# Performance work log

Hardware: AMD Instinct MI355X
Metric: run time of the kernel (lower is better)

Reference implementation:

```python
import jax, jax.numpy as jnp
import numpy as np


def setup_inputs() -> dict:
    key = jax.random.key(0)
    k1, k2 = jax.random.split(key)
    x = jax.random.normal(k1, (32, 128, 56, 56), dtype=jnp.float32)
    weight = jax.random.normal(k2, (256, 128, 3, 3), dtype=jnp.float32) * 0.01
    bias = jnp.zeros((256,), dtype=jnp.float32)
    return {"x": x, "weight": weight, "bias": bias}


def reference(x, weight, bias):
    # Faithful to Conv2dGEMM: im2col + GEMM is mathematically a standard
    # cross-correlation conv with the given stride/padding. We express it as
    # the efficient fused form (implicit GEMM) which computes identical math.
    stride, padding = 1, 1
    out = jax.lax.conv_general_dilated(
        x, weight,
        window_strides=(stride, stride),
        padding=[(padding, padding), (padding, padding)],
        dimension_numbers=("NCHW", "OIHW", "NCHW"),
    )  # [B, out_ch, H_out, W_out]
    return out + bias[None, :, None, None]
```

## Files before the change

kernel.cpp:

```cpp
#include <hip/hip_runtime.h>
#include <stdint.h>

typedef __bf16 bf16x8 __attribute__((ext_vector_type(8)));
typedef float  f32x4  __attribute__((ext_vector_type(4)));

#define NB   32
#define CI   128
#define HH   56
#define WW   56
#define CO   256
#define HP   58
#define HW   (HH*WW)
#define MTOT (NB*HW)
#define KTOT 1152

#define XT_ELEMS ((size_t)NB*HP*HP*CI)
#define XT_BYTES (XT_ELEMS*2)
#define WT_BYTES ((size_t)CO*KTOT*2)
#define CTR_OFF  (XT_BYTES + WT_BYTES)

#define XPOSE_BLOCKS (NB*HH)
#define WX_BLOCKS    ((CO*KTOT)/256)
#define HALO_BLOCKS  ((NB*228*16)/256)

__global__ void prep_kernel(const float* __restrict__ x, const float* __restrict__ wg,
                            __bf16* __restrict__ xt, __bf16* __restrict__ wt,
                            unsigned* __restrict__ ctr) {
  __shared__ float tile[CI][57];
  int bx = blockIdx.x, t = threadIdx.x;
  if (bx == 0 && t == 0) *ctr = 0u;
  if (bx < XPOSE_BLOCKS) {
    int n = bx / HH, h = bx % HH;
    const float* src = x + (size_t)n * CI * HW + (size_t)h * WW;
    for (int idx = t; idx < CI * 14; idx += 256) {
      int c = idx / 14, w4 = idx - c * 14;
      float4 v = *(const float4*)(src + (size_t)c * HW + w4 * 4);
      tile[c][w4 * 4 + 0] = v.x;
      tile[c][w4 * 4 + 1] = v.y;
      tile[c][w4 * 4 + 2] = v.z;
      tile[c][w4 * 4 + 3] = v.w;
    }
    __syncthreads();
    __bf16* dst = xt + ((size_t)(n * HP + h + 1) * HP + 1) * CI;
    for (int idx = t; idx < WW * 16; idx += 256) {
      int w = idx >> 4, c8 = (idx & 15) * 8;
      bf16x8 v;
      for (int k = 0; k < 8; ++k) v[k] = (__bf16)tile[c8 + k][w];
      *(bf16x8*)(dst + (size_t)w * CI + c8) = v;
    }
  } else if (bx < XPOSE_BLOCKS + WX_BLOCKS) {
    int id = (bx - XPOSE_BLOCKS) * 256 + t;
    int o = id / KTOT;
    int k = id - o * KTOT;
    int rs = k >> 7, c = k & 127;
    wt[id] = (__bf16)wg[(size_t)o * KTOT + c * 9 + rs];
  } else {
    int id = (bx - XPOSE_BLOCKS - WX_BLOCKS) * 256 + t;
    int chunk = id & 15;
    int p = (id >> 4) % 228;
    int n = id / (228 * 16);
    int h, w;
    if (p < 58)       { h = 0;           w = p; }
    else if (p < 116) { h = 57;          w = p - 58; }
    else if (p < 172) { h = p - 116 + 1; w = 0; }
    else              { h = p - 172 + 1; w = 57; }
    int4* dst = (int4*)(xt + ((size_t)(n * HP + h) * HP + w) * CI) + chunk;
    *dst = make_int4(0, 0, 0, 0);
  }
}

#define BM 128
#define BN 256
#define NKT 18
#define NTILES (MTOT/BM)

#define STAGE_A2(BS, OFF) \
  { _Pragma("unroll") for (int i_ = 0; i_ < 2; ++i_) \
      __builtin_amdgcn_global_load_lds( \
        (const __attribute__((address_space(1))) void*)(xtc + baseA[i_] + (OFF)), \
        (__attribute__((address_space(3))) void*)(lds + (BS)*16384 + i_*8192 + ldst), 16, 0, 0); }

#define STAGE_B01(BS, OFF) \
  { _Pragma("unroll") for (int i_ = 0; i_ < 2; ++i_) \
      __builtin_amdgcn_global_load_lds( \
        (const __attribute__((address_space(1))) void*)(wtc + baseB[i_] + (OFF)), \
        (__attribute__((address_space(3))) void*)(lds + 49152 + (BS)*32768 + i_*8192 + ldst), 16, 0, 0); }

#define STAGE_B23(BS, OFF) \
  { _Pragma("unroll") for (int i_ = 2; i_ < 4; ++i_) \
      __builtin_amdgcn_global_load_lds( \
        (const __attribute__((address_space(1))) void*)(wtc + baseB[i_] + (OFF)), \
        (__attribute__((address_space(3))) void*)(lds + 49152 + (BS)*32768 + i_*8192 + ldst), 16, 0, 0); }

#define KBODY(KT, BC, BS, DOSTAGE, DOBAR, VMCLIT) do { \
  int kt2_ = (KT) + 2; \
  int rs2_ = kt2_ >> 1; int r2_ = (rs2_*11) >> 5; int s2_ = rs2_ - 3*r2_; \
  uint32_t offA2_ = (uint32_t)((r2_*HP + s2_) * 256 + (kt2_ & 1) * 128); \
  uint32_t offB2_ = (uint32_t)(kt2_ * 128); \
  const char* Ab_ = lds + (BC)*16384; \
  const char* Bb_ = lds + 49152 + (BC)*32768; \
  bf16x8 av_[4][2], bva_[2][2], bvb_[2][2]; \
  _Pragma("unroll") for (int a_ = 0; a_ < 4; ++a_) { \
    av_[a_][0] = *(const bf16x8*)(Ab_ + rowA + a_*2048 + slot0); \
    av_[a_][1] = *(const bf16x8*)(Ab_ + rowA + a_*2048 + slot1); } \
  _Pragma("unroll") for (int b_ = 0; b_ < 2; ++b_) { \
    bva_[b_][0] = *(const bf16x8*)(Bb_ + rowB + b_*2048 + slot0); \
    bva_[b_][1] = *(const bf16x8*)(Bb_ + rowB + b_*2048 + slot1); } \
  if (DOSTAGE) { STAGE_A2(BS, offA2_); STAGE_B01(BS, offB2_); } \
  __builtin_amdgcn_s_setprio(1); \
  _Pragma("unroll") for (int a_ = 0; a_ < 4; ++a_) { \
    _Pragma("unroll") for (int b_ = 0; b_ < 2; ++b_) { \
      acc[a_][b_] = __builtin_amdgcn_mfma_f32_16x16x32_bf16(av_[a_][0], bva_[b_][0], acc[a_][b_], 0, 0, 0); \
      acc[a_][b_] = __builtin_amdgcn_mfma_f32_16x16x32_bf16(av_[a_][1], bva_[b_][1], acc[a_][b_], 0, 0, 0); } } \
  __builtin_amdgcn_s_setprio(0); \
  _Pragma("unroll") for (int b_ = 0; b_ < 2; ++b_) { \
    bvb_[b_][0] = *(const bf16x8*)(Bb_ + rowB + 4096 + b_*2048 + slot0); \
    bvb_[b_][1] = *(const bf16x8*)(Bb_ + rowB + 4096 + b_*2048 + slot1); } \
  if (DOSTAGE) { STAGE_B23(BS, offB2_); } \
  __builtin_amdgcn_s_setprio(1); \
  _Pragma("unroll") for (int a_ = 0; a_ < 4; ++a_) { \
    _Pragma("unroll") for (int b_ = 0; b_ < 2; ++b_) { \
      acc[a_][b_+2] = __builtin_amdgcn_mfma_f32_16x16x32_bf16(av_[a_][0], bvb_[b_][0], acc[a_][b_+2], 0, 0, 0); \
      acc[a_][b_+2] = __builtin_amdgcn_mfma_f32_16x16x32_bf16(av_[a_][1], bvb_[b_][1], acc[a_][b_+2], 0, 0, 0); } } \
  __builtin_amdgcn_s_setprio(0); \
  if (DOBAR) { \
    asm volatile("s_waitcnt vmcnt(" VMCLIT ")" ::: "memory"); \
    __builtin_amdgcn_sched_barrier(0); \
    __builtin_amdgcn_s_barrier(); \
    __builtin_amdgcn_sched_barrier(0); } \
} while (0)

__global__ __launch_bounds__(512, 2) void conv_gemm(
    const __bf16* __restrict__ xt, const __bf16* __restrict__ wt,
    const float* __restrict__ bias, float* __restrict__ out,
    unsigned* __restrict__ ctr) {
  __shared__ char lds[147456];
  __shared__ int sh_mb;
  int t = threadIdx.x;
  const char* xtc = (const char*)xt;
  const char* wtc = (const char*)wt;

  int arow = t >> 3;
  int kbsrc = ((t & 7) * 16) ^ ((arow & 7) << 4);
  int ldst = t * 16;
  uint32_t baseB[4];
#pragma unroll
  for (int i = 0; i < 4; ++i)
    baseB[i] = (i * 64 + arow) * (KTOT * 2) + kbsrc;

  int wid = t >> 6, lane = t & 63;
  int wm = (wid >> 2) * 64;
  int wn = (wid & 3) * 64;
  int lr = lane & 15, hi = lane >> 4;
  int swz = (lr & 7) << 4;
  int slot0 = (hi * 16) ^ swz;
  int slot1 = (64 + hi * 16) ^ swz;
  int rowA = (wm + lr) * 128;
  int rowB = (wn + lr) * 128;

  for (;;) {
    if (t == 0) sh_mb = (int)atomicAdd(ctr, 1u);
    __syncthreads();
    int mb = sh_mb;
    if (mb >= NTILES) break;

    uint32_t baseA[2];
#pragma unroll
    for (int i = 0; i < 2; ++i) {
      unsigned m = mb * BM + i * 64 + arow;
      unsigned nimg = m / HW;
      unsigned hw = m - nimg * HW;
      unsigned h = hw / WW;
      unsigned w = hw - h * WW;
      baseA[i] = ((nimg * HP + h) * HP + w) * (CI * 2) + kbsrc;
    }

    f32x4 acc[4][4];
#pragma unroll
    for (int i = 0; i < 4; ++i)
#pragma unroll
      for (int j = 0; j < 4; ++j) acc[i][j] = (f32x4){0.f, 0.f, 0.f, 0.f};

    STAGE_A2(0, 0u);   STAGE_B01(0, 0u);   STAGE_B23(0, 0u);
    STAGE_A2(1, 128u); STAGE_B01(1, 128u); STAGE_B23(1, 128u);
    asm volatile("s_waitcnt vmcnt(6)" ::: "memory");
    __builtin_amdgcn_sched_barrier(0);
    __builtin_amdgcn_s_barrier();
    __builtin_amdgcn_sched_barrier(0);

    for (int kt = 0; kt < 15; kt += 3) {
      KBODY(kt + 0, 0, 2, 1, 1, "6");
      KBODY(kt + 1, 1, 0, 1, 1, "6");
      KBODY(kt + 2, 2, 1, 1, 1, "6");
    }
    KBODY(15, 0, 2, 1, 1, "6");
    KBODY(16, 1, 0, 0, 1, "0");
    KBODY(17, 2, 1, 0, 0, "0");

#pragma unroll
    for (int j = 0; j < 4; ++j) {
      int o = wn + j * 16 + lr;
      float bv = bias[o];
#pragma unroll
      for (int i = 0; i < 4; ++i) {
        unsigned m0 = mb * BM + wm + i * 16 + hi * 4;
        unsigned nimg = m0 / HW;
        unsigned hw = m0 - nimg * HW;
        f32x4 v = acc[i][j];
        v[0] += bv; v[1] += bv; v[2] += bv; v[3] += bv;
        *(f32x4*)(out + ((size_t)nimg * CO + o) * HW + hw) = v;
      }
    }
  }
}

extern "C" void kernel_launch(void* const* d_in, const int* in_sizes, int n_in,
                              void* d_out, int out_size, void* d_ws, size_t ws_size,
                              hipStream_t stream) {
  const float* x    = (const float*)d_in[0];
  const float* wg   = (const float*)d_in[1];
  const float* bias = (const float*)d_in[2];
  float* out = (float*)d_out;

  __bf16* xt = (__bf16*)d_ws;
  __bf16* wt = (__bf16*)((char*)d_ws + XT_BYTES);
  unsigned* ctr = (unsigned*)((char*)d_ws + CTR_OFF);

  prep_kernel<<<XPOSE_BLOCKS + WX_BLOCKS + HALO_BLOCKS, 256, 0, stream>>>(x, wg, xt, wt, ctr);
  conv_gemm<<<256, 512, 0, stream>>>(xt, wt, bias, out, ctr);
}
```

Measured before the change: 218.8 us.

## Prefetch next persistent tile's first K stages during current tile's tail

Moves the atomic tile fetch ahead so the next tile index is known during the current tile's main loop. The last two K iterations then stage the next tile's first two K slices into LDS, removing the pipeline drain and refill bubble between persistent tiles. The K loop is fully unrolled with compile-time offsets. The cost is more code size and register pressure, plus reliance on barrier ordering, since sh_nx is written without a dedicated sync before it is read.

Measured after the change: 304.8 us. +39.3%, slower.

```diff
diff --git a/kernel.cpp b/kernel.cpp
--- a/kernel.cpp
+++ b/kernel.cpp
@@ -74,10 +74,15 @@
 #define NKT 18
 #define NTILES (MTOT/BM)
 
-#define STAGE_A2(BS, OFF) \
+__device__ __forceinline__ uint32_t offA_of(int kt) {
+  int rs = kt >> 1; int r = (rs * 11) >> 5; int s = rs - 3 * r;
+  return (uint32_t)((r * HP + s) * 256 + (kt & 1) * 128);
+}
+
+#define STAGE_A2(BS, OFF, AB) \
   { _Pragma("unroll") for (int i_ = 0; i_ < 2; ++i_) \
       __builtin_amdgcn_global_load_lds( \
-        (const __attribute__((address_space(1))) void*)(xtc + baseA[i_] + (OFF)), \
+        (const __attribute__((address_space(1))) void*)(xtc + (AB)[i_] + (OFF)), \
         (__attribute__((address_space(3))) void*)(lds + (BS)*16384 + i_*8192 + ldst), 16, 0, 0); }
 
 #define STAGE_B01(BS, OFF) \
@@ -92,11 +97,8 @@
         (const __attribute__((address_space(1))) void*)(wtc + baseB[i_] + (OFF)), \
         (__attribute__((address_space(3))) void*)(lds + 49152 + (BS)*32768 + i_*8192 + ldst), 16, 0, 0); }
 
-#define KBODY(KT, BC, BS, DOSTAGE, DOBAR, VMCLIT) do { \
-  int kt2_ = (KT) + 2; \
-  int rs2_ = kt2_ >> 1; int r2_ = (rs2_*11) >> 5; int s2_ = rs2_ - 3*r2_; \
-  uint32_t offA2_ = (uint32_t)((r2_*HP + s2_) * 256 + (kt2_ & 1) * 128); \
-  uint32_t offB2_ = (uint32_t)(kt2_ * 128); \
+#define KBODY(BC, BS, DOSTAGE, DOBAR, VMCLIT, AB, OA, OB) do { \
+  uint32_t offA2_ = (OA), offB2_ = (OB); \
   const char* Ab_ = lds + (BC)*16384; \
   const char* Bb_ = lds + 49152 + (BC)*32768; \
   bf16x8 av_[4][2], bva_[2][2], bvb_[2][2]; \
@@ -106,7 +108,7 @@
   _Pragma("unroll") for (int b_ = 0; b_ < 2; ++b_) { \
     bva_[b_][0] = *(const bf16x8*)(Bb_ + rowB + b_*2048 + slot0); \
     bva_[b_][1] = *(const bf16x8*)(Bb_ + rowB + b_*2048 + slot1); } \
-  if (DOSTAGE) { STAGE_A2(BS, offA2_); STAGE_B01(BS, offB2_); } \
+  if (DOSTAGE) { STAGE_A2(BS, offA2_, AB); STAGE_B01(BS, offB2_); } \
   __builtin_amdgcn_s_setprio(1); \
   _Pragma("unroll") for (int a_ = 0; a_ < 4; ++a_) { \
     _Pragma("unroll") for (int b_ = 0; b_ < 2; ++b_) { \
@@ -130,12 +132,21 @@
     __builtin_amdgcn_sched_barrier(0); } \
 } while (0)
 
+#define CALC_BASEA(DST, MB) \
+  { _Pragma("unroll") for (int i_ = 0; i_ < 2; ++i_) { \
+      unsigned m_ = (unsigned)(MB) * BM + i_ * 64 + arow; \
+      unsigned nimg_ = m_ / HW; \
+      unsigned hw_ = m_ - nimg_ * HW; \
+      unsigned h_ = hw_ / WW; \
+      unsigned w_ = hw_ - h_ * WW; \
+      (DST)[i_] = ((nimg_ * HP + h_) * HP + w_) * (CI * 2) + kbsrc; } }
+
 __global__ __launch_bounds__(512, 2) void conv_gemm(
     const __bf16* __restrict__ xt, const __bf16* __restrict__ wt,
     const float* __restrict__ bias, float* __restrict__ out,
     unsigned* __restrict__ ctr) {
   __shared__ char lds[147456];
-  __shared__ int sh_mb;
+  __shared__ int sh_mb, sh_nx;
   int t = threadIdx.x;
   const char* xtc = (const char*)xt;
   const char* wtc = (const char*)wt;
@@ -158,22 +169,23 @@
   int rowA = (wm + lr) * 128;
   int rowB = (wn + lr) * 128;
 
+  if (t == 0) sh_mb = (int)atomicAdd(ctr, 1u);
+  __syncthreads();
+  int mb = sh_mb;
+  if (mb >= NTILES) return;
+
+  uint32_t baseA[2], baseN[2];
+  CALC_BASEA(baseA, mb);
+
+  STAGE_A2(0, 0u, baseA); STAGE_B01(0, 0u);   STAGE_B23(0, 0u);
+  STAGE_A2(1, 128u, baseA); STAGE_B01(1, 128u); STAGE_B23(1, 128u);
+  asm volatile("s_waitcnt vmcnt(6)" ::: "memory");
+  __builtin_amdgcn_sched_barrier(0);
+  __builtin_amdgcn_s_barrier();
+  __builtin_amdgcn_sched_barrier(0);
+
   for (;;) {
-    if (t == 0) sh_mb = (int)atomicAdd(ctr, 1u);
-    __syncthreads();
-    int mb = sh_mb;
-    if (mb >= NTILES) break;
-
-    uint32_t baseA[2];
-#pragma unroll
-    for (int i = 0; i < 2; ++i) {
-      unsigned m = mb * BM + i * 64 + arow;
-      unsigned nimg = m / HW;
-      unsigned hw = m - nimg * HW;
-      unsigned h = hw / WW;
-      unsigned w = hw - h * WW;
-      baseA[i] = ((nimg * HP + h) * HP + w) * (CI * 2) + kbsrc;
-    }
+    if (t == 0) sh_nx = (int)atomicAdd(ctr, 1u);
 
     f32x4 acc[4][4];
 #pragma unroll
@@ -181,21 +193,25 @@
 #pragma unroll
       for (int j = 0; j < 4; ++j) acc[i][j] = (f32x4){0.f, 0.f, 0.f, 0.f};
 
-    STAGE_A2(0, 0u);   STAGE_B01(0, 0u);   STAGE_B23(0, 0u);
-    STAGE_A2(1, 128u); STAGE_B01(1, 128u); STAGE_B23(1, 128u);
-    asm volatile("s_waitcnt vmcnt(6)" ::: "memory");
-    __builtin_amdgcn_sched_barrier(0);
-    __builtin_amdgcn_s_barrier();
-    __builtin_amdgcn_sched_barrier(0);
-
+#pragma unroll
     for (int kt = 0; kt < 15; kt += 3) {
-      KBODY(kt + 0, 0, 2, 1, 1, "6");
-      KBODY(kt + 1, 1, 0, 1, 1, "6");
-      KBODY(kt + 2, 2, 1, 1, 1, "6");
-    }
-    KBODY(15, 0, 2, 1, 1, "6");
-    KBODY(16, 1, 0, 0, 1, "0");
-    KBODY(17, 2, 1, 0, 0, "0");
+      KBODY(0, 2, 1, 1, "6", baseA, offA_of(kt + 2), (uint32_t)((kt + 2) * 128));
+      KBODY(1, 0, 1, 1, "6", baseA, offA_of(kt + 3), (uint32_t)((kt + 3) * 128));
+      KBODY(2, 1, 1, 1, "6", baseA, offA_of(kt + 4), (uint32_t)((kt + 4) * 128));
+    }
+    KBODY(0, 2, 1, 1, "6", baseA, offA_of(17), (uint32_t)(17 * 128));
+
+    int nx = sh_nx;
+    bool have = nx < NTILES;
+    CALC_BASEA(baseN, nx);
+
+    if (have) {
+      KBODY(1, 0, 1, 1, "6", baseN, 0u, 0u);
+      KBODY(2, 1, 1, 1, "6", baseN, 128u, 128u);
+    } else {
+      KBODY(1, 0, 0, 1, "0", baseA, 0u, 0u);
+      KBODY(2, 1, 0, 0, "0", baseA, 0u, 0u);
+    }
 
 #pragma unroll
     for (int j = 0; j < 4; ++j) {
@@ -203,7 +219,7 @@
       float bv = bias[o];
 #pragma unroll
       for (int i = 0; i < 4; ++i) {
-        unsigned m0 = mb * BM + wm + i * 16 + hi * 4;
+        unsigned m0 = (unsigned)mb * BM + wm + i * 16 + hi * 4;
         unsigned nimg = m0 / HW;
         unsigned hw = m0 - nimg * HW;
         f32x4 v = acc[i][j];
@@ -211,6 +227,10 @@
         *(f32x4*)(out + ((size_t)nimg * CO + o) * HW + hw) = v;
       }
     }
+
+    if (!have) break;
+    mb = nx;
+    baseA[0] = baseN[0]; baseA[1] = baseN[1];
   }
 }
 
```
